# Performance work log

Hardware: AMD Instinct MI355X
Metric: run time of the kernel (lower is better)

Reference implementation:

```python
import jax, jax.numpy as jnp
import numpy as np

N, E = 50000, 800000
IN_DIM, HEADS, OUT_DIM = 256, 8, 32
NEG_SLOPE = 0.2  # PyG GATConv default leaky_relu slope
LN_EPS = 1e-5


def setup_inputs() -> dict:
    key = jax.random.key(0)
    ks = jax.random.split(key, 8)
    HC = HEADS * OUT_DIM
    x = jax.random.normal(ks[0], (N, IN_DIM), dtype=jnp.float32)
    edge_index = jax.random.randint(ks[1], (2, E), 0, N, dtype=jnp.int32)
    # GATConv params: lin (no bias), att_src/att_dst [H,C], output bias [H*C]
    W = jax.random.normal(ks[2], (IN_DIM, HC), dtype=jnp.float32) / np.sqrt(IN_DIM)
    att_src = jax.random.normal(ks[3], (HEADS, OUT_DIM), dtype=jnp.float32) / np.sqrt(OUT_DIM)
    att_dst = jax.random.normal(ks[4], (HEADS, OUT_DIM), dtype=jnp.float32) / np.sqrt(OUT_DIM)
    bias = jnp.zeros((HC,), dtype=jnp.float32)
    ln_gamma = jnp.ones((HC,), dtype=jnp.float32)
    ln_beta = jnp.zeros((HC,), dtype=jnp.float32)
    return {"x": x, "edge_index": edge_index, "W": W, "att_src": att_src,
            "att_dst": att_dst, "bias": bias, "ln_gamma": ln_gamma, "ln_beta": ln_beta}


def reference(x, edge_index, W, att_src, att_dst, bias, ln_gamma, ln_beta):
    n = x.shape[0]
    # GATConv adds self-loops by default
    loop = jnp.arange(n, dtype=edge_index.dtype)
    src = jnp.concatenate([edge_index[0], loop])  # [E+N]
    dst = jnp.concatenate([edge_index[1], loop])
    h = (x @ W).reshape(n, HEADS, OUT_DIM)              # [N,H,C]
    a_src = jnp.einsum('nhc,hc->nh', h, att_src)        # [N,H]
    a_dst = jnp.einsum('nhc,hc->nh', h, att_dst)
    e = jax.nn.leaky_relu(a_src[src] + a_dst[dst], NEG_SLOPE)  # [E+N,H]
    # segment-softmax over incoming edges of each destination node
    m = jax.ops.segment_max(e, dst, num_segments=n)
    e = jnp.exp(e - m[dst])
    denom = jax.ops.segment_sum(e, dst, num_segments=n)
    alpha = e / (denom[dst] + 1e-16)                    # [E+N,H]
    out = jax.ops.segment_sum(h[src] * alpha[:, :, None], dst, num_segments=n)
    out = out.reshape(n, HEADS * OUT_DIM) + bias        # concat heads + bias
    # LayerNorm(out_dim*heads); dropout is identity in eval
    mu = jnp.mean(out, axis=-1, keepdims=True)
    var = jnp.mean(jnp.square(out - mu), axis=-1, keepdims=True)
    return ln_gamma * (out - mu) * jax.lax.rsqrt(var + LN_EPS) + ln_beta
```

## Files before the change

### kernel.cpp

```cpp
#include <hip/hip_runtime.h>
#include <hip/hip_bf16.h>

#define HEADS 8
#define OUT_DIM 32
#define HC 256
#define IN_DIM 256
#define NEG_SLOPE 0.2f
#define LN_EPS 1e-5f
#define CAP 64

typedef __attribute__((ext_vector_type(8))) short bf16x8;
typedef __attribute__((ext_vector_type(4))) float f32x4;
typedef __attribute__((ext_vector_type(2))) float f32x2;

__device__ __forceinline__ unsigned short f2bf(float f) {
    unsigned int u = __float_as_uint(f);
    unsigned int r = u + 0x7FFFu + ((u >> 16) & 1u);
    return (unsigned short)(r >> 16);
}
__device__ __forceinline__ unsigned short f2bf_hw(float f) {
    union { __hip_bfloat16 h; unsigned short u; } c;
    c.h = __float2bfloat16(f);
    return c.u;
}
__device__ __forceinline__ bf16x8 pack8(const float4 a, const float4 b) {
    bf16x8 r;
    r[0] = (short)f2bf_hw(a.x); r[1] = (short)f2bf_hw(a.y);
    r[2] = (short)f2bf_hw(a.z); r[3] = (short)f2bf_hw(a.w);
    r[4] = (short)f2bf_hw(b.x); r[5] = (short)f2bf_hw(b.y);
    r[6] = (short)f2bf_hw(b.z); r[7] = (short)f2bf_hw(b.w);
    return r;
}

__global__ __launch_bounds__(256) void prep0(const float* __restrict__ W,
                                             unsigned short* __restrict__ Wt,
                                             const float* __restrict__ X,
                                             unsigned short* __restrict__ Xb,
                                             int* __restrict__ cnt,
                                             int N, int nXb) {
    const int b = blockIdx.x;
    const int t = threadIdx.x;
    if (b < 16) {
        __shared__ float tile[64][65];
        const int n0 = (b & 3) * 64;
        const int k0 = (b >> 2) * 64;
        const int r = t >> 4;
        const int c = (t & 15) * 4;
#pragma unroll
        for (int j = 0; j < 4; j++) {
            const int kl = r + j * 16;
            const float4 v = *(const float4*)(W + (size_t)(k0 + kl) * HC + n0 + c);
            tile[kl][c + 0] = v.x; tile[kl][c + 1] = v.y;
            tile[kl][c + 2] = v.z; tile[kl][c + 3] = v.w;
        }
        __syncthreads();
#pragma unroll
        for (int j = 0; j < 4; j++) {
            const int nr = r + j * 16;
            ushort4 o;
            o.x = f2bf(tile[c + 0][nr]);
            o.y = f2bf(tile[c + 1][nr]);
            o.z = f2bf(tile[c + 2][nr]);
            o.w = f2bf(tile[c + 3][nr]);
            *(ushort4*)(Wt + (size_t)(n0 + nr) * IN_DIM + k0 + c) = o;
        }
    } else if (b < 16 + nXb) {
        const size_t i = ((size_t)(b - 16) * 256 + t) * 8;
        if (i < (size_t)N * IN_DIM) {
            const float4 v0 = *(const float4*)(X + i);
            const float4 v1 = *(const float4*)(X + i + 4);
            *(bf16x8*)(Xb + i) = pack8(v0, v1);
        }
    } else {
        const int idx = (b - 16 - nXb) * 256 + t;
        if (idx < N) cnt[idx] = 0;
    }
}

__global__ __launch_bounds__(256) void gemm_sc(const unsigned short* __restrict__ Xb,
                                               const unsigned short* __restrict__ Wt,
                                               unsigned short* __restrict__ Hb,
                                               const float* __restrict__ att_s,
                                               const float* __restrict__ att_d,
                                               float* __restrict__ a_s,
                                               float* __restrict__ a_d,
                                               const int* __restrict__ ei,
                                               int* __restrict__ cnt,
                                               unsigned short* __restrict__ bucket,
                                               int E, int N) {
    const int b = blockIdx.x;
    const int t = threadIdx.x;
    const int nTiles = (N + 63) >> 6;
    const int nSc = (E + N + 511) >> 9;
    const int g = b >> 1;

    if (!(b & 1) && g < nTiles) {
        const int w = t >> 6, lane = t & 63;
        const int l16 = lane & 15, quad = lane >> 4;
        const int m0 = g * 64;
        const int n0 = w * 64;

        const unsigned short* ap[4];
#pragma unroll
        for (int mi = 0; mi < 4; mi++) {
            const int gm = m0 + mi * 16 + l16;
            ap[mi] = Xb + (size_t)(gm < N ? gm : 0) * IN_DIM + quad * 8;
        }
        const unsigned short* bp[4];
#pragma unroll
        for (int ni = 0; ni < 4; ni++)
            bp[ni] = Wt + (size_t)(n0 + ni * 16 + l16) * IN_DIM + quad * 8;

        f32x4 acc[4][4] = {};
#pragma unroll
        for (int k0 = 0; k0 < IN_DIM; k0 += 32) {
            bf16x8 af[4], bfr[4];
#pragma unroll
            for (int mi = 0; mi < 4; mi++) af[mi]  = *(const bf16x8*)(ap[mi] + k0);
#pragma unroll
            for (int ni = 0; ni < 4; ni++) bfr[ni] = *(const bf16x8*)(bp[ni] + k0);
#pragma unroll
            for (int ni = 0; ni < 4; ni++)
#pragma unroll
                for (int mi = 0; mi < 4; mi++)
                    acc[mi][ni] = __builtin_amdgcn_mfma_f32_16x16x32_bf16(af[mi], bfr[ni], acc[mi][ni], 0, 0, 0);
        }

        {
            float as_v[4], ad_v[4];
#pragma unroll
            for (int ni = 0; ni < 4; ni++) {
                as_v[ni] = att_s[n0 + ni * 16 + l16];
                ad_v[ni] = att_d[n0 + ni * 16 + l16];
            }
#pragma unroll
            for (int mi = 0; mi < 4; mi++) {
#pragma unroll
                for (int reg = 0; reg < 4; reg++) {
                    float ps0 = acc[mi][0][reg] * as_v[0] + acc[mi][1][reg] * as_v[1];
                    float ps1 = acc[mi][2][reg] * as_v[2] + acc[mi][3][reg] * as_v[3];
                    float pd0 = acc[mi][0][reg] * ad_v[0] + acc[mi][1][reg] * ad_v[1];
                    float pd1 = acc[mi][2][reg] * ad_v[2] + acc[mi][3][reg] * ad_v[3];
#pragma unroll
                    for (int m = 1; m <= 2; m <<= 1) {
                        ps0 += __shfl_xor(ps0, m); ps1 += __shfl_xor(ps1, m);
                        pd0 += __shfl_xor(pd0, m); pd1 += __shfl_xor(pd1, m);
                    }
                    const int s2 = l16 & 3;
                    float v = s2 == 0 ? ps0 : (s2 == 1 ? ps1 : (s2 == 2 ? pd0 : pd1));
                    v += __shfl_xor(v, 4); v += __shfl_xor(v, 8);
                    const int gm = m0 + mi * 16 + quad * 4 + reg;
                    if (l16 < 4 && gm < N) {
                        float* dst = (l16 >= 2) ? a_d : a_s;
                        dst[(size_t)gm * HEADS + 2 * w + (l16 & 1)] = v;
                    }
                }
            }
        }

#pragma unroll
        for (int mi = 0; mi < 4; mi++) {
#pragma unroll
            for (int reg = 0; reg < 4; reg++) {
                const int gm = m0 + mi * 16 + quad * 4 + reg;
                if (gm < N) {
#pragma unroll
                    for (int ni = 0; ni < 4; ni++)
                        Hb[(size_t)gm * HC + n0 + ni * 16 + l16] = f2bf_hw(acc[mi][ni][reg]);
                }
            }
        }
    } else {
        const int sc = b - min((b + 1) >> 1, nTiles);
        if (sc >= nSc) return;
        const int ebase = sc << 9;
#pragma unroll
        for (int r = 0; r < 2; r++) {
            const int e = ebase + (r << 8) + t;
            if (e < E + N) {
                int s, d;
                if (e < E) { s = ei[e]; d = ei[E + e]; }
                else       { s = d = e - E; }
                int slot = atomicAdd(&cnt[d], 1);
                if (slot < CAP) bucket[(size_t)d * CAP + slot] = (unsigned short)s;
            }
        }
    }
}

__global__ __launch_bounds__(256) void csr_agg(const int* __restrict__ cntArr,
                                               const unsigned short* __restrict__ bucket,
                                               const unsigned short* __restrict__ Hb,
                                               const float* __restrict__ a_s,
                                               const float* __restrict__ a_d,
                                               const float* __restrict__ bias,
                                               const float* __restrict__ gamma,
                                               const float* __restrict__ beta,
                                               float* __restrict__ out, int N) {
    const int lane = threadIdx.x & 63;
    const int node = blockIdx.x * 4 + (threadIdx.x >> 6);
    if (node >= N) return;
    const int half = lane >> 5;
    const int sl   = lane & 31;
    const int c0   = sl * 8;
    const int hh   = sl >> 2;
    const size_t base = (size_t)node * CAP;
    const int cnt  = min(cntArr[node], CAP);
    const float adv = a_d[(size_t)node * HEADS + hh];
    const int breg = (int)bucket[base + lane];

    f32x2 acc2[4] = {};
    float wsum = 0.f;
    const int nIter = (cnt + 15) >> 4;

    float tl[8]; float msk[8]; uint4 hv[8];
#pragma unroll
    for (int j = 0; j < 8; j++) {
        const int idx = 2 * j + half;
        const int s = __shfl(breg, idx & 63);
        const bool ok = idx < cnt;
        const int sv = ok ? s : 0;
        msk[j] = ok ? 1.f : 0.f;
        tl[j] = a_s[(size_t)sv * HEADS + hh];
        hv[j] = *(const uint4*)(Hb + (size_t)sv * HC + c0);
    }

    for (int it = 0; it < nIter; ++it) {
        float tl2[8]; float msk2[8]; uint4 hv2[8];
        const int i2 = (it + 1) * 16;
#pragma unroll
        for (int j = 0; j < 8; j++) {
            const int idx = i2 + 2 * j + half;
            const int s = __shfl(breg, idx & 63);
            const bool ok = idx < cnt;
            const int sv = ok ? s : 0;
            msk2[j] = ok ? 1.f : 0.f;
            tl2[j] = a_s[(size_t)sv * HEADS + hh];
            hv2[j] = *(const uint4*)(Hb + (size_t)sv * HC + c0);
        }
#pragma unroll
        for (int j = 0; j < 8; j++) {
            const float tt = tl[j] + adv;
            const float l = fmaxf(tt, NEG_SLOPE * tt);
            const float ww = msk[j] * __expf(l);
            wsum += ww;
            f32x2 wv; wv.x = ww; wv.y = ww;
            f32x2 p0, p1, p2, p3;
            p0.x = __uint_as_float(hv[j].x << 16); p0.y = __uint_as_float(hv[j].x & 0xffff0000u);
            p1.x = __uint_as_float(hv[j].y << 16); p1.y = __uint_as_float(hv[j].y & 0xffff0000u);
            p2.x = __uint_as_float(hv[j].z << 16); p2.y = __uint_as_float(hv[j].z & 0xffff0000u);
            p3.x = __uint_as_float(hv[j].w << 16); p3.y = __uint_as_float(hv[j].w & 0xffff0000u);
            acc2[0] += wv * p0;
            acc2[1] += wv * p1;
            acc2[2] += wv * p2;
            acc2[3] += wv * p3;
        }
#pragma unroll
        for (int j = 0; j < 8; j++) { tl[j] = tl2[j]; msk[j] = msk2[j]; hv[j] = hv2[j]; }
    }

    float acc[8];
    acc[0] = acc2[0].x; acc[1] = acc2[0].y; acc[2] = acc2[1].x; acc[3] = acc2[1].y;
    acc[4] = acc2[2].x; acc[5] = acc2[2].y; acc[6] = acc2[3].x; acc[7] = acc2[3].y;

#pragma unroll
    for (int k = 0; k < 8; k++) acc[k] += __shfl_xor(acc[k], 32);
    wsum += __shfl_xor(wsum, 32);

    const float inv = 1.f / (wsum + 1e-16f);
    const float4 b0 = *(const float4*)(bias + c0);
    const float4 b1 = *(const float4*)(bias + c0 + 4);
    float v[8];
    v[0] = acc[0] * inv + b0.x; v[1] = acc[1] * inv + b0.y;
    v[2] = acc[2] * inv + b0.z; v[3] = acc[3] * inv + b0.w;
    v[4] = acc[4] * inv + b1.x; v[5] = acc[5] * inv + b1.y;
    v[6] = acc[6] * inv + b1.z; v[7] = acc[7] * inv + b1.w;

    float s1 = v[0] + v[1] + v[2] + v[3] + v[4] + v[5] + v[6] + v[7];
#pragma unroll
    for (int m = 1; m < 64; m <<= 1) s1 += __shfl_xor(s1, m);
    const float mu = s1 * (1.f / 512.f);
    float d[8];
    float sq = 0.f;
#pragma unroll
    for (int k = 0; k < 8; k++) { d[k] = v[k] - mu; sq += d[k] * d[k]; }
#pragma unroll
    for (int m = 1; m < 64; m <<= 1) sq += __shfl_xor(sq, m);
    const float rs = rsqrtf(sq * (1.f / 512.f) + LN_EPS);

    const float e0 = half ? d[4] : d[0];
    const float e1 = half ? d[5] : d[1];
    const float e2 = half ? d[6] : d[2];
    const float e3 = half ? d[7] : d[3];
    const int co = c0 + half * 4;
    const float4 g  = *(const float4*)(gamma + co);
    const float4 be = *(const float4*)(beta + co);
    float4 o;
    o.x = g.x * e0 * rs + be.x;
    o.y = g.y * e1 * rs + be.y;
    o.z = g.z * e2 * rs + be.z;
    o.w = g.w * e3 * rs + be.w;
    *(float4*)(out + (size_t)node * HC + co) = o;
}

extern "C" void kernel_launch(void* const* d_in, const int* in_sizes, int n_in,
                              void* d_out, int out_size, void* d_ws, size_t ws_size,
                              hipStream_t stream) {
    const float* x     = (const float*)d_in[0];
    const int*   ei    = (const int*)d_in[1];
    const float* W     = (const float*)d_in[2];
    const float* att_s = (const float*)d_in[3];
    const float* att_d = (const float*)d_in[4];
    const float* bias  = (const float*)d_in[5];
    const float* gamma = (const float*)d_in[6];
    const float* beta  = (const float*)d_in[7];
    float* out = (float*)d_out;

    const int N = in_sizes[0] / IN_DIM;
    const int E = in_sizes[1] / 2;

    unsigned short* Hb = (unsigned short*)d_ws;
    unsigned short* Wt = Hb + (size_t)N * HC;
    unsigned short* Xb = Wt + (size_t)IN_DIM * HC;
    float* a_s  = (float*)(Xb + (size_t)N * IN_DIM);
    float* a_d  = a_s + (size_t)N * HEADS;
    int* cnt    = (int*)(a_d + (size_t)N * HEADS);
    unsigned short* bucket = (unsigned short*)(cnt + N);

    const int nXb = (int)(((size_t)N * IN_DIM / 8 + 255) / 256);
    const int nZe = (N + 255) / 256;
    prep0<<<16 + nXb + nZe, 256, 0, stream>>>(W, Wt, x, Xb, cnt, N, nXb);

    const int nTiles = (N + 63) / 64;
    const int nSc = (E + N + 511) / 512;
    gemm_sc<<<nTiles + nSc, 256, 0, stream>>>(Xb, Wt, Hb, att_s, att_d, a_s, a_d,
                                              ei, cnt, bucket, E, N);

    csr_agg<<<(N + 3) / 4, 256, 0, stream>>>(cnt, bucket, Hb, a_s, a_d,
                                             bias, gamma, beta, out, N);
}
```

Before: 263.2 us.

## Make GEMM blocks persistent over 8 row tiles and move self-loop init into prep

Each GEMM block now keeps its whole W^T slice in registers and loops over 8 row tiles. This cuts the block count and the repeated W loads. Self-loop edges are written during the counter-init pass, so the scatter blocks only handle real edges, at 1024 edges per block. The interleaving of GEMM and scatter blocks changes from 1:1 to 1:7. Holding W in registers raises register pressure and lowers occupancy, and the GEMM part now has far fewer blocks to spread across the CUs.

```diff
diff --git a/kernel.cpp b/kernel.cpp
--- a/kernel.cpp
+++ b/kernel.cpp
@@ -8,6 +8,7 @@
 #define NEG_SLOPE 0.2f
 #define LN_EPS 1e-5f
 #define CAP 64
+#define MT 8
 
 typedef __attribute__((ext_vector_type(8))) short bf16x8;
 typedef __attribute__((ext_vector_type(4))) float f32x4;
@@ -37,6 +38,7 @@
                                              const float* __restrict__ X,
                                              unsigned short* __restrict__ Xb,
                                              int* __restrict__ cnt,
+                                             unsigned short* __restrict__ bucket,
                                              int N, int nXb) {
     const int b = blockIdx.x;
     const int t = threadIdx.x;
@@ -73,7 +75,10 @@
         }
     } else {
         const int idx = (b - 16 - nXb) * 256 + t;
-        if (idx < N) cnt[idx] = 0;
+        if (idx < N) {
+            cnt[idx] = 1;
+            bucket[(size_t)idx * CAP] = (unsigned short)idx;
+        }
     }
 }
 
@@ -91,48 +96,55 @@
     const int b = blockIdx.x;
     const int t = threadIdx.x;
     const int nTiles = (N + 63) >> 6;
-    const int nSc = (E + N + 511) >> 9;
-    const int g = b >> 1;
-
-    if (!(b & 1) && g < nTiles) {
+    const int nGemm = (nTiles + MT - 1) / MT;
+    const int nSc = (E + 1023) >> 10;
+
+    if (((b & 7) == 7) && ((b >> 3) < nGemm)) {
+        const int gb = b >> 3;
         const int w = t >> 6, lane = t & 63;
         const int l16 = lane & 15, quad = lane >> 4;
-        const int m0 = g * 64;
         const int n0 = w * 64;
 
-        const unsigned short* ap[4];
-#pragma unroll
-        for (int mi = 0; mi < 4; mi++) {
-            const int gm = m0 + mi * 16 + l16;
-            ap[mi] = Xb + (size_t)(gm < N ? gm : 0) * IN_DIM + quad * 8;
-        }
-        const unsigned short* bp[4];
-#pragma unroll
-        for (int ni = 0; ni < 4; ni++)
-            bp[ni] = Wt + (size_t)(n0 + ni * 16 + l16) * IN_DIM + quad * 8;
-
-        f32x4 acc[4][4] = {};
-#pragma unroll
-        for (int k0 = 0; k0 < IN_DIM; k0 += 32) {
-            bf16x8 af[4], bfr[4];
-#pragma unroll
-            for (int mi = 0; mi < 4; mi++) af[mi]  = *(const bf16x8*)(ap[mi] + k0);
-#pragma unroll
-            for (int ni = 0; ni < 4; ni++) bfr[ni] = *(const bf16x8*)(bp[ni] + k0);
-#pragma unroll
-            for (int ni = 0; ni < 4; ni++)
-#pragma unroll
-                for (int mi = 0; mi < 4; mi++)
-                    acc[mi][ni] = __builtin_amdgcn_mfma_f32_16x16x32_bf16(af[mi], bfr[ni], acc[mi][ni], 0, 0, 0);
-        }
-
-        {
-            float as_v[4], ad_v[4];
-#pragma unroll
-            for (int ni = 0; ni < 4; ni++) {
-                as_v[ni] = att_s[n0 + ni * 16 + l16];
-                ad_v[ni] = att_d[n0 + ni * 16 + l16];
-            }
+        bf16x8 B[4][8];
+#pragma unroll
+        for (int ni = 0; ni < 4; ni++) {
+            const unsigned short* bp = Wt + (size_t)(n0 + ni * 16 + l16) * IN_DIM + quad * 8;
+#pragma unroll
+            for (int ks = 0; ks < 8; ks++)
+                B[ni][ks] = *(const bf16x8*)(bp + ks * 32);
+        }
+        float as_v[4], ad_v[4];
+#pragma unroll
+        for (int ni = 0; ni < 4; ni++) {
+            as_v[ni] = att_s[n0 + ni * 16 + l16];
+            ad_v[ni] = att_d[n0 + ni * 16 + l16];
+        }
+
+        for (int mt = 0; mt < MT; mt++) {
+            const int tileId = gb * MT + mt;
+            if (tileId >= nTiles) break;
+            const int m0 = tileId * 64;
+
+            const unsigned short* ap[4];
+#pragma unroll
+            for (int mi = 0; mi < 4; mi++) {
+                const int gm = m0 + mi * 16 + l16;
+                ap[mi] = Xb + (size_t)(gm < N ? gm : 0) * IN_DIM + quad * 8;
+            }
+
+            f32x4 acc[4][4] = {};
+#pragma unroll
+            for (int ks = 0; ks < 8; ks++) {
+                bf16x8 af[4];
+#pragma unroll
+                for (int mi = 0; mi < 4; mi++) af[mi] = *(const bf16x8*)(ap[mi] + ks * 32);
+#pragma unroll
+                for (int ni = 0; ni < 4; ni++)
+#pragma unroll
+                    for (int mi = 0; mi < 4; mi++)
+                        acc[mi][ni] = __builtin_amdgcn_mfma_f32_16x16x32_bf16(af[mi], B[ni][ks], acc[mi][ni], 0, 0, 0);
+            }
+
 #pragma unroll
             for (int mi = 0; mi < 4; mi++) {
 #pragma unroll
@@ -156,31 +168,32 @@
                     }
                 }
             }
-        }
-
-#pragma unroll
-        for (int mi = 0; mi < 4; mi++) {
-#pragma unroll
-            for (int reg = 0; reg < 4; reg++) {
-                const int gm = m0 + mi * 16 + quad * 4 + reg;
-                if (gm < N) {
-#pragma unroll
-                    for (int ni = 0; ni < 4; ni++)
-                        Hb[(size_t)gm * HC + n0 + ni * 16 + l16] = f2bf_hw(acc[mi][ni][reg]);
+
+#pragma unroll
+            for (int mi = 0; mi < 4; mi++) {
+#pragma unroll
+                for (int reg = 0; reg < 4; reg++) {
+                    const int gm = m0 + mi * 16 + quad * 4 + reg;
+                    if (gm < N) {
+#pragma unroll
+                        for (int ni = 0; ni < 4; ni++)
+                            Hb[(size_t)gm * HC + n0 + ni * 16 + l16] = f2bf_hw(acc[mi][ni][reg]);
+                    }
                 }
             }
         }
     } else {
-        const int sc = b - min((b + 1) >> 1, nTiles);
+        const int nGemmBefore = min((b + 1) >> 3, (E + 1023) >> 10 >= 0 ? ((nTiles + MT - 1) / MT) : 0);
+        const int sc = b - min((b + 1) >> 3, nGemm);
+        (void)nGemmBefore;
         if (sc >= nSc) return;
-        const int ebase = sc << 9;
-#pragma unroll
-        for (int r = 0; r < 2; r++) {
+        const int ebase = sc << 10;
+#pragma unroll
+        for (int r = 0; r < 4; r++) {
             const int e = ebase + (r << 8) + t;
-            if (e < E + N) {
-                int s, d;
-                if (e < E) { s = ei[e]; d = ei[E + e]; }
-                else       { s = d = e - E; }
+            if (e < E) {
+                const int s = ei[e];
+                const int d = ei[E + e];
                 int slot = atomicAdd(&cnt[d], 1);
                 if (slot < CAP) bucket[(size_t)d * CAP + slot] = (unsigned short)s;
             }
@@ -329,12 +342,13 @@
 
     const int nXb = (int)(((size_t)N * IN_DIM / 8 + 255) / 256);
     const int nZe = (N + 255) / 256;
-    prep0<<<16 + nXb + nZe, 256, 0, stream>>>(W, Wt, x, Xb, cnt, N, nXb);
+    prep0<<<16 + nXb + nZe, 256, 0, stream>>>(W, Wt, x, Xb, cnt, bucket, N, nXb);
 
     const int nTiles = (N + 63) / 64;
-    const int nSc = (E + N + 511) / 512;
-    gemm_sc<<<nTiles + nSc, 256, 0, stream>>>(Xb, Wt, Hb, att_s, att_d, a_s, a_d,
-                                              ei, cnt, bucket, E, N);
+    const int nGemm = (nTiles + MT - 1) / MT;
+    const int nSc = (E + 1023) / 1024;
+    gemm_sc<<<nGemm + nSc, 256, 0, stream>>>(Xb, Wt, Hb, att_s, att_d, a_s, a_d,
+                                             ei, cnt, bucket, E, N);
 
     csr_agg<<<(N + 3) / 4, 256, 0, stream>>>(cnt, bucket, Hb, a_s, a_d,
                                              bias, gamma, beta, out, N);
```

Measured after the change: 472.1 us. 1.79x slower.
